# Optimization experiments

Hardware: AMD Instinct MI355X
Metric: run time of the kernel (lower is better)

Reference implementation:

```python
import jax, jax.numpy as jnp
import numpy as np

N = 200000   # active voxels
D = 80       # dense grid side
K = 27       # 3x3x3 kernel offsets
CIN, CMID, COUT = 16, 32, 32
EPS = 1e-3   # BatchNorm1d eps from the module


def _build_rulebook():
    """Submanifold conv rulebook: for each kernel offset, (input_idx, output_idx) pairs.
    Padded to length N with dummy output index N (scatter target discarded)."""
    rng = np.random.default_rng(0)
    lin = rng.choice(D ** 3, size=N, replace=False)
    coords = np.stack(np.unravel_index(lin, (D, D, D)), axis=1).astype(np.int64)  # [N,3]
    lookup = np.full(D ** 3, -1, np.int64)
    lookup[lin] = np.arange(N)
    rule_in = np.zeros((K, N), np.int32)
    rule_out = np.full((K, N), N, np.int32)  # dummy row N = padding
    k = 0
    for dx in (-1, 0, 1):
        for dy in (-1, 0, 1):
            for dz in (-1, 0, 1):
                nb = coords + np.array([dx, dy, dz])
                valid = np.all((nb >= 0) & (nb < D), axis=1)
                nb_lin = (nb[valid, 0] * D + nb[valid, 1]) * D + nb[valid, 2]
                idx = lookup[nb_lin]
                hit = idx >= 0
                src = idx[hit].astype(np.int32)
                dst = np.nonzero(valid)[0][hit].astype(np.int32)
                m = src.shape[0]
                rule_in[k, :m] = src
                rule_out[k, :m] = dst
                k += 1
    return rule_in, rule_out


def setup_inputs() -> dict:
    key = jax.random.key(0)
    ks = jax.random.split(key, 3)
    ri, ro = _build_rulebook()
    return {
        "feats": jax.random.normal(ks[0], (N, CIN), jnp.float32),
        "W1": jax.random.normal(ks[1], (K, CIN, CMID), jnp.float32) * 0.05,
        "gamma1": jnp.ones((CMID,), jnp.float32),
        "beta1": jnp.zeros((CMID,), jnp.float32),
        "W2": jax.random.normal(ks[2], (K, CMID, COUT), jnp.float32) * 0.05,
        "gamma2": jnp.ones((COUT,), jnp.float32),
        "beta2": jnp.zeros((COUT,), jnp.float32),
        "rule_in": jnp.asarray(ri),
        "rule_out": jnp.asarray(ro),
    }


def _subm_conv(feats, W, rule_in, rule_out):
    """Gather-GEMM-scatter over kernel offsets (lax.scan keeps one offset resident)."""
    n = feats.shape[0]

    def step(acc, xs):
        in_i, out_i, Wk = xs
        return acc.at[out_i].add(feats[in_i] @ Wk), None

    acc0 = jnp.zeros((n + 1, W.shape[-1]), feats.dtype)  # row n is padding sink
    acc, _ = jax.lax.scan(step, acc0, (rule_in, rule_out, W))
    return acc[:n]


def _bn_relu(x, gamma, beta):
    # BatchNorm1d training-mode forward (biased var) + ReLU
    mu = x.mean(0)
    var = jnp.mean((x - mu) ** 2, 0)
    return jax.nn.relu((x - mu) * jax.lax.rsqrt(var + EPS) * gamma + beta)


def reference(feats, W1, gamma1, beta1, W2, gamma2, beta2, rule_in, rule_out):
    x = _bn_relu(_subm_conv(feats, W1, rule_in, rule_out), gamma1, beta1)
    x = _bn_relu(_subm_conv(x, W2, rule_in, rule_out), gamma2, beta2)
    return x
```

## Files before the change

kernel.cpp:

```cpp
#include <hip/hip_runtime.h>

#define NVOX 200000
#define KOFF 27
#define CIN 16
#define CMID 32
#define COUT 32
#define EPSBN 1e-3f

typedef _Float16 f16x8 __attribute__((ext_vector_type(8)));
typedef _Float16 f16x4 __attribute__((ext_vector_type(4)));
typedef float f32x16 __attribute__((ext_vector_type(16)));

#define OFF_X1H 21600000
#define OFF_FH  34400064
#define OFF_WB1 40800096
#define OFF_WB2 40827744
#define OFF_ST  40883040

__global__ __launch_bounds__(256) void k_build(const int* __restrict__ rule_in,
                                               const int* __restrict__ rule_out,
                                               const float* __restrict__ feats,
                                               const float* __restrict__ W1,
                                               const float* __restrict__ W2,
                                               int* __restrict__ gatherT,
                                               _Float16* __restrict__ featsh,
                                               _Float16* __restrict__ WB1,
                                               _Float16* __restrict__ WB2,
                                               _Float16* __restrict__ x1h) {
  int e = blockIdx.x * 256 + threadIdx.x;
  if (e < KOFF * NVOX) {
    int k = e / NVOX;
    int dst = rule_out[e];
    if (dst < NVOX) gatherT[k * NVOX + dst] = rule_in[e];
  }
  if (e < NVOX * CIN / 4) {
    float4 f = ((const float4*)feats)[e];
    f16x4 h = {(_Float16)f.x, (_Float16)f.y, (_Float16)f.z, (_Float16)f.w};
    ((f16x4*)featsh)[e] = h;
  }
  if (e < KOFF * 512) {
    int j = e & 7, l = (e >> 3) & 63, k = e >> 9;
    int kk = ((l >> 5) << 3) + j;
    int n = l & 31;
    WB1[e] = (_Float16)W1[(k * CIN + kk) * CMID + n];
  }
  if (e < KOFF * 1024) {
    int j = e & 7, l = (e >> 3) & 63, f = (e >> 9) & 1, k = e >> 10;
    int kk = (f << 4) + ((l >> 5) << 3) + j;
    int n = l & 31;
    WB2[e] = (_Float16)W2[(k * CMID + kk) * COUT + n];
  }
  if (e < CMID) x1h[(size_t)NVOX * CMID + e] = (_Float16)0.f;
  if (e < CIN) featsh[(size_t)NVOX * CIN + e] = (_Float16)0.f;
}

__global__ __launch_bounds__(512, 4) void k_conv1m(const _Float16* __restrict__ featsh,
                                                   const int* __restrict__ gatherT,
                                                   const uint4* __restrict__ WB1,
                                                   _Float16* __restrict__ x1h,
                                                   float* __restrict__ gsums) {
  __shared__ uint4 wlds[KOFF * 64];
  __shared__ float lsum[64];
  int tid = threadIdx.x;
  for (int i = tid; i < KOFF * 64; i += 512) wlds[i] = WB1[i];
  if (tid < 64) lsum[tid] = 0.f;
  __syncthreads();

  int lane = tid & 63, wave = tid >> 6;
  int m = lane & 31, khalf = lane >> 5;
  int rowbase = blockIdx.x * 256 + wave * 32;
  int row = rowbase + m;
  int rowc = (row < NVOX) ? row : (NVOX - 1);

  int idx[KOFF];
#pragma unroll
  for (int k = 0; k < KOFF; ++k) idx[k] = gatherT[k * NVOX + rowc];

  f32x16 c;
#pragma unroll
  for (int i = 0; i < 16; ++i) c[i] = 0.f;

#pragma unroll
  for (int k = 0; k < KOFF; ++k) {
    unsigned s = ((unsigned)idx[k] < (unsigned)NVOX) ? (unsigned)idx[k] : (unsigned)NVOX;
    f16x8 a = *(const f16x8*)(featsh + (size_t)s * CIN + (khalf << 3));
    f16x8 b = ((const f16x8*)wlds)[k * 64 + lane];
    c = __builtin_amdgcn_mfma_f32_32x32x16_f16(a, b, c, 0, 0, 0);
  }

  float s0 = 0.f, q0 = 0.f;
#pragma unroll
  for (int r = 0; r < 16; ++r) {
    int grow = rowbase + (r & 3) + ((r >> 2) << 3) + (khalf << 2);
    float mk = (grow < NVOX) ? 1.f : 0.f;
    float v = c[r] * mk;
    s0 += v; q0 += v * v;
    if (grow < NVOX) x1h[(size_t)grow * CMID + m] = (_Float16)c[r];
  }
  s0 += __shfl_xor(s0, 32, 64);
  q0 += __shfl_xor(q0, 32, 64);
  if (lane < 32) {
    atomicAdd(&lsum[m], s0);
    atomicAdd(&lsum[32 + m], q0);
  }
  __syncthreads();
  if (tid < 64) atomicAdd(&gsums[tid], lsum[tid]);
}

__global__ __launch_bounds__(256) void k_bnrelu1h(_Float16* __restrict__ x1h,
                                                  const float* __restrict__ sums,
                                                  const float* __restrict__ gamma,
                                                  const float* __restrict__ beta) {
  int t = blockIdx.x * 256 + threadIdx.x;
  if (t >= NVOX * CMID / 8) return;
  int c = (t & 3) * 8;
  const float inv_n = 1.0f / (float)NVOX;
  float sc[8], sh[8];
#pragma unroll
  for (int i = 0; i < 8; ++i) {
    float mu = sums[c + i] * inv_n;
    float var = sums[32 + c + i] * inv_n - mu * mu;
    float s = gamma[c + i] * rsqrtf(var + EPSBN);
    sc[i] = s; sh[i] = beta[c + i] - mu * s;
  }
  f16x8* p = (f16x8*)x1h + t;
  f16x8 v = *p;
#pragma unroll
  for (int i = 0; i < 8; ++i) {
    float x = fmaf((float)v[i], sc[i], sh[i]);
    v[i] = (_Float16)fmaxf(x, 0.f);
  }
  *p = v;
}

__global__ __launch_bounds__(512, 4) void k_conv2m(const _Float16* __restrict__ x1h,
                                                   const int* __restrict__ gatherT,
                                                   const uint4* __restrict__ WB2,
                                                   float* __restrict__ out,
                                                   float* __restrict__ gsums) {
  __shared__ uint4 wlds[KOFF * 128];
  __shared__ float lsum[64];
  int tid = threadIdx.x;
  for (int i = tid; i < KOFF * 128; i += 512) wlds[i] = WB2[i];
  if (tid < 64) lsum[tid] = 0.f;
  __syncthreads();

  int lane = tid & 63, wave = tid >> 6;
  int m = lane & 31, khalf = lane >> 5;
  int rowbase = blockIdx.x * 256 + wave * 32;
  int row = rowbase + m;
  int rowc = (row < NVOX) ? row : (NVOX - 1);

  int idx[KOFF];
#pragma unroll
  for (int k = 0; k < KOFF; ++k) idx[k] = gatherT[k * NVOX + rowc];

  f32x16 c;
#pragma unroll
  for (int i = 0; i < 16; ++i) c[i] = 0.f;

#pragma unroll
  for (int k = 0; k < KOFF; ++k) {
    unsigned s = ((unsigned)idx[k] < (unsigned)NVOX) ? (unsigned)idx[k] : (unsigned)NVOX;
    const _Float16* rp = x1h + (size_t)s * CMID + (khalf << 3);
    f16x8 a0 = *(const f16x8*)(rp);
    f16x8 a1 = *(const f16x8*)(rp + 16);
    f16x8 b0 = ((const f16x8*)wlds)[(k * 2 + 0) * 64 + lane];
    f16x8 b1 = ((const f16x8*)wlds)[(k * 2 + 1) * 64 + lane];
    c = __builtin_amdgcn_mfma_f32_32x32x16_f16(a0, b0, c, 0, 0, 0);
    c = __builtin_amdgcn_mfma_f32_32x32x16_f16(a1, b1, c, 0, 0, 0);
  }

  float s0 = 0.f, q0 = 0.f;
#pragma unroll
  for (int r = 0; r < 16; ++r) {
    int grow = rowbase + (r & 3) + ((r >> 2) << 3) + (khalf << 2);
    float mk = (grow < NVOX) ? 1.f : 0.f;
    float v = c[r] * mk;
    s0 += v; q0 += v * v;
    if (grow < NVOX) out[(size_t)grow * COUT + m] = c[r];
  }
  s0 += __shfl_xor(s0, 32, 64);
  q0 += __shfl_xor(q0, 32, 64);
  if (lane < 32) {
    atomicAdd(&lsum[m], s0);
    atomicAdd(&lsum[32 + m], q0);
  }
  __syncthreads();
  if (tid < 64) atomicAdd(&gsums[tid], lsum[tid]);
}

__global__ __launch_bounds__(256) void k_bnrelu2(float* __restrict__ out,
                                                 const float* __restrict__ sums,
                                                 const float* __restrict__ gamma,
                                                 const float* __restrict__ beta) {
  int t = blockIdx.x * 256 + threadIdx.x;
  if (t >= NVOX * COUT / 4) return;
  int c = (t & 7) * 4;
  const float inv_n = 1.0f / (float)NVOX;
  float sc[4], sh[4];
#pragma unroll
  for (int i = 0; i < 4; ++i) {
    float mu = sums[c + i] * inv_n;
    float var = sums[32 + c + i] * inv_n - mu * mu;
    float s = gamma[c + i] * rsqrtf(var + EPSBN);
    sc[i] = s; sh[i] = beta[c + i] - mu * s;
  }
  float4* p = (float4*)out + t;
  float4 v = *p;
  v.x = fmaxf(fmaf(v.x, sc[0], sh[0]), 0.f);
  v.y = fmaxf(fmaf(v.y, sc[1], sh[1]), 0.f);
  v.z = fmaxf(fmaf(v.z, sc[2], sh[2]), 0.f);
  v.w = fmaxf(fmaf(v.w, sc[3], sh[3]), 0.f);
  *p = v;
}

extern "C" void kernel_launch(void* const* d_in, const int* in_sizes, int n_in,
                              void* d_out, int out_size, void* d_ws, size_t ws_size,
                              hipStream_t stream) {
  const float* feats  = (const float*)d_in[0];
  const float* W1     = (const float*)d_in[1];
  const float* gamma1 = (const float*)d_in[2];
  const float* beta1  = (const float*)d_in[3];
  const float* W2     = (const float*)d_in[4];
  const float* gamma2 = (const float*)d_in[5];
  const float* beta2  = (const float*)d_in[6];
  const int* rule_in  = (const int*)d_in[7];
  const int* rule_out = (const int*)d_in[8];
  float* out = (float*)d_out;

  int*       gatherT = (int*)d_ws;
  _Float16*  x1h     = (_Float16*)((char*)d_ws + OFF_X1H);
  _Float16*  featsh  = (_Float16*)((char*)d_ws + OFF_FH);
  _Float16*  WB1     = (_Float16*)((char*)d_ws + OFF_WB1);
  _Float16*  WB2     = (_Float16*)((char*)d_ws + OFF_WB2);
  float*     stats   = (float*)((char*)d_ws + OFF_ST);

  hipMemsetAsync(gatherT, 0xFF, (size_t)KOFF * NVOX * 4, stream);
  hipMemsetAsync(stats, 0, 128 * 4, stream);
  k_build<<<(KOFF * NVOX + 255) / 256, 256, 0, stream>>>(
      rule_in, rule_out, feats, W1, W2, gatherT, featsh, WB1, WB2, x1h);
  k_conv1m<<<782, 512, 0, stream>>>(featsh, gatherT, (const uint4*)WB1, x1h, stats);
  k_bnrelu1h<<<(NVOX * CMID / 8 + 255) / 256, 256, 0, stream>>>(x1h, stats, gamma1, beta1);
  k_conv2m<<<782, 512, 0, stream>>>(x1h, gatherT, (const uint4*)WB2, out, stats + 64);
  k_bnrelu2<<<(NVOX * COUT / 4 + 255) / 256, 256, 0, stream>>>(out, stats + 64, gamma2, beta2);
}
```

Measured before the change: 217.3 us.

## Fuse BN1+ReLU into conv2 gather, prefetch gathers, drop memsets

The first BatchNorm+ReLU pass is folded into conv2: it applies per-channel scale and shift in fp16 to the gathered rows and masks invalid neighbours, so the separate elementwise kernel and its read/write of x1h go away. Both conv kernels now prefetch gathered rows three offsets ahead through a small register ring, to hide gather latency. The memset of gatherT is replaced by filling -1 gaps in the build kernel, which assumes rule_out is sorted, and the stats memset moves into the build kernel as well. The costs are that the BN is recomputed 27 times per row in fp16, and the conv kernels need more registers.

```diff
diff --git a/kernel.cpp b/kernel.cpp
--- a/kernel.cpp
+++ b/kernel.cpp
@@ -26,12 +26,21 @@
                                                _Float16* __restrict__ featsh,
                                                _Float16* __restrict__ WB1,
                                                _Float16* __restrict__ WB2,
-                                               _Float16* __restrict__ x1h) {
+                                               float* __restrict__ stats) {
   int e = blockIdx.x * 256 + threadIdx.x;
   if (e < KOFF * NVOX) {
     int k = e / NVOX;
+    int pos = e - k * NVOX;
     int dst = rule_out[e];
-    if (dst < NVOX) gatherT[k * NVOX + dst] = rule_in[e];
+    int ndst = (pos == NVOX - 1) ? NVOX : rule_out[e + 1];
+    int* __restrict__ gk = gatherT + k * NVOX;
+    if (dst < NVOX) {
+      gk[dst] = rule_in[e];
+      if (pos == 0) {
+        for (int d = 0; d < dst; ++d) gk[d] = -1;
+      }
+      for (int d = dst + 1; d < ndst; ++d) gk[d] = -1;
+    }
   }
   if (e < NVOX * CIN / 4) {
     float4 f = ((const float4*)feats)[e];
@@ -50,8 +59,8 @@
     int n = l & 31;
     WB2[e] = (_Float16)W2[(k * CMID + kk) * COUT + n];
   }
-  if (e < CMID) x1h[(size_t)NVOX * CMID + e] = (_Float16)0.f;
   if (e < CIN) featsh[(size_t)NVOX * CIN + e] = (_Float16)0.f;
+  if (e < 128) stats[e] = 0.f;
 }
 
 __global__ __launch_bounds__(512, 4) void k_conv1m(const _Float16* __restrict__ featsh,
@@ -67,7 +76,7 @@
   __syncthreads();
 
   int lane = tid & 63, wave = tid >> 6;
-  int m = lane & 31, khalf = lane >> 5;
+  int m = lane & 31, h = lane >> 5;
   int rowbase = blockIdx.x * 256 + wave * 32;
   int row = rowbase + m;
   int rowc = (row < NVOX) ? row : (NVOX - 1);
@@ -76,14 +85,24 @@
 #pragma unroll
   for (int k = 0; k < KOFF; ++k) idx[k] = gatherT[k * NVOX + rowc];
 
+  f16x8 A[3];
+#pragma unroll
+  for (int p = 0; p < 3; ++p) {
+    unsigned s = ((unsigned)idx[p] < (unsigned)NVOX) ? (unsigned)idx[p] : (unsigned)NVOX;
+    A[p] = *(const f16x8*)(featsh + (size_t)s * CIN + (h << 3));
+  }
+
   f32x16 c;
 #pragma unroll
   for (int i = 0; i < 16; ++i) c[i] = 0.f;
 
 #pragma unroll
   for (int k = 0; k < KOFF; ++k) {
-    unsigned s = ((unsigned)idx[k] < (unsigned)NVOX) ? (unsigned)idx[k] : (unsigned)NVOX;
-    f16x8 a = *(const f16x8*)(featsh + (size_t)s * CIN + (khalf << 3));
+    f16x8 a = A[k % 3];
+    if (k + 3 < KOFF) {
+      unsigned s = ((unsigned)idx[k + 3] < (unsigned)NVOX) ? (unsigned)idx[k + 3] : (unsigned)NVOX;
+      A[k % 3] = *(const f16x8*)(featsh + (size_t)s * CIN + (h << 3));
+    }
     f16x8 b = ((const f16x8*)wlds)[k * 64 + lane];
     c = __builtin_amdgcn_mfma_f32_32x32x16_f16(a, b, c, 0, 0, 0);
   }
@@ -91,7 +110,7 @@
   float s0 = 0.f, q0 = 0.f;
 #pragma unroll
   for (int r = 0; r < 16; ++r) {
-    int grow = rowbase + (r & 3) + ((r >> 2) << 3) + (khalf << 2);
+    int grow = rowbase + (r & 3) + ((r >> 2) << 3) + (h << 2);
     float mk = (grow < NVOX) ? 1.f : 0.f;
     float v = c[r] * mk;
     s0 += v; q0 += v * v;
@@ -107,35 +126,12 @@
   if (tid < 64) atomicAdd(&gsums[tid], lsum[tid]);
 }
 
-__global__ __launch_bounds__(256) void k_bnrelu1h(_Float16* __restrict__ x1h,
-                                                  const float* __restrict__ sums,
-                                                  const float* __restrict__ gamma,
-                                                  const float* __restrict__ beta) {
-  int t = blockIdx.x * 256 + threadIdx.x;
-  if (t >= NVOX * CMID / 8) return;
-  int c = (t & 3) * 8;
-  const float inv_n = 1.0f / (float)NVOX;
-  float sc[8], sh[8];
-#pragma unroll
-  for (int i = 0; i < 8; ++i) {
-    float mu = sums[c + i] * inv_n;
-    float var = sums[32 + c + i] * inv_n - mu * mu;
-    float s = gamma[c + i] * rsqrtf(var + EPSBN);
-    sc[i] = s; sh[i] = beta[c + i] - mu * s;
-  }
-  f16x8* p = (f16x8*)x1h + t;
-  f16x8 v = *p;
-#pragma unroll
-  for (int i = 0; i < 8; ++i) {
-    float x = fmaf((float)v[i], sc[i], sh[i]);
-    v[i] = (_Float16)fmaxf(x, 0.f);
-  }
-  *p = v;
-}
-
 __global__ __launch_bounds__(512, 4) void k_conv2m(const _Float16* __restrict__ x1h,
                                                    const int* __restrict__ gatherT,
                                                    const uint4* __restrict__ WB2,
+                                                   const float* __restrict__ sums1,
+                                                   const float* __restrict__ gamma1,
+                                                   const float* __restrict__ beta1,
                                                    float* __restrict__ out,
                                                    float* __restrict__ gsums) {
   __shared__ uint4 wlds[KOFF * 128];
@@ -146,35 +142,75 @@
   __syncthreads();
 
   int lane = tid & 63, wave = tid >> 6;
-  int m = lane & 31, khalf = lane >> 5;
+  int m = lane & 31, h = lane >> 5;
   int rowbase = blockIdx.x * 256 + wave * 32;
   int row = rowbase + m;
   int rowc = (row < NVOX) ? row : (NVOX - 1);
 
+  const float inv_n = 1.0f / (float)NVOX;
+  f16x8 sc0, sh0, sc1, sh1;
+#pragma unroll
+  for (int i = 0; i < 8; ++i) {
+    int c0 = 8 * h + i;
+    float mu = sums1[c0] * inv_n;
+    float var = sums1[32 + c0] * inv_n - mu * mu;
+    float s = gamma1[c0] * rsqrtf(var + EPSBN);
+    sc0[i] = (_Float16)s; sh0[i] = (_Float16)(beta1[c0] - mu * s);
+    int c1 = 16 + 8 * h + i;
+    mu = sums1[c1] * inv_n;
+    var = sums1[32 + c1] * inv_n - mu * mu;
+    s = gamma1[c1] * rsqrtf(var + EPSBN);
+    sc1[i] = (_Float16)s; sh1[i] = (_Float16)(beta1[c1] - mu * s);
+  }
+
   int idx[KOFF];
 #pragma unroll
   for (int k = 0; k < KOFF; ++k) idx[k] = gatherT[k * NVOX + rowc];
 
+  f16x8 A0[3], A1[3];
+#pragma unroll
+  for (int p = 0; p < 3; ++p) {
+    unsigned s = ((unsigned)idx[p] < (unsigned)NVOX) ? (unsigned)idx[p] : 0u;
+    const _Float16* rp = x1h + (size_t)s * CMID + (h << 3);
+    A0[p] = *(const f16x8*)rp;
+    A1[p] = *(const f16x8*)(rp + 16);
+  }
+
   f32x16 c;
 #pragma unroll
   for (int i = 0; i < 16; ++i) c[i] = 0.f;
 
+  const _Float16 zero_h = (_Float16)0.f;
 #pragma unroll
   for (int k = 0; k < KOFF; ++k) {
-    unsigned s = ((unsigned)idx[k] < (unsigned)NVOX) ? (unsigned)idx[k] : (unsigned)NVOX;
-    const _Float16* rp = x1h + (size_t)s * CMID + (khalf << 3);
-    f16x8 a0 = *(const f16x8*)(rp);
-    f16x8 a1 = *(const f16x8*)(rp + 16);
+    _Float16 mk = ((unsigned)idx[k] < (unsigned)NVOX) ? (_Float16)1.f : zero_h;
+    f16x8 a0 = A0[k % 3], a1 = A1[k % 3];
+    f16x8 y0, y1;
+#pragma unroll
+    for (int i = 0; i < 8; ++i) {
+      _Float16 t0 = a0[i] * sc0[i] + sh0[i];
+      t0 = (t0 > zero_h) ? t0 : zero_h;
+      y0[i] = t0 * mk;
+      _Float16 t1 = a1[i] * sc1[i] + sh1[i];
+      t1 = (t1 > zero_h) ? t1 : zero_h;
+      y1[i] = t1 * mk;
+    }
+    if (k + 3 < KOFF) {
+      unsigned s = ((unsigned)idx[k + 3] < (unsigned)NVOX) ? (unsigned)idx[k + 3] : 0u;
+      const _Float16* rp = x1h + (size_t)s * CMID + (h << 3);
+      A0[k % 3] = *(const f16x8*)rp;
+      A1[k % 3] = *(const f16x8*)(rp + 16);
+    }
     f16x8 b0 = ((const f16x8*)wlds)[(k * 2 + 0) * 64 + lane];
     f16x8 b1 = ((const f16x8*)wlds)[(k * 2 + 1) * 64 + lane];
-    c = __builtin_amdgcn_mfma_f32_32x32x16_f16(a0, b0, c, 0, 0, 0);
-    c = __builtin_amdgcn_mfma_f32_32x32x16_f16(a1, b1, c, 0, 0, 0);
+    c = __builtin_amdgcn_mfma_f32_32x32x16_f16(y0, b0, c, 0, 0, 0);
+    c = __builtin_amdgcn_mfma_f32_32x32x16_f16(y1, b1, c, 0, 0, 0);
   }
 
   float s0 = 0.f, q0 = 0.f;
 #pragma unroll
   for (int r = 0; r < 16; ++r) {
-    int grow = rowbase + (r & 3) + ((r >> 2) << 3) + (khalf << 2);
+    int grow = rowbase + (r & 3) + ((r >> 2) << 3) + (h << 2);
     float mk = (grow < NVOX) ? 1.f : 0.f;
     float v = c[r] * mk;
     s0 += v; q0 += v * v;
@@ -236,12 +272,10 @@
   _Float16*  WB2     = (_Float16*)((char*)d_ws + OFF_WB2);
   float*     stats   = (float*)((char*)d_ws + OFF_ST);
 
-  hipMemsetAsync(gatherT, 0xFF, (size_t)KOFF * NVOX * 4, stream);
-  hipMemsetAsync(stats, 0, 128 * 4, stream);
   k_build<<<(KOFF * NVOX + 255) / 256, 256, 0, stream>>>(
-      rule_in, rule_out, feats, W1, W2, gatherT, featsh, WB1, WB2, x1h);
+      rule_in, rule_out, feats, W1, W2, gatherT, featsh, WB1, WB2, stats);
   k_conv1m<<<782, 512, 0, stream>>>(featsh, gatherT, (const uint4*)WB1, x1h, stats);
-  k_bnrelu1h<<<(NVOX * CMID / 8 + 255) / 256, 256, 0, stream>>>(x1h, stats, gamma1, beta1);
-  k_conv2m<<<782, 512, 0, stream>>>(x1h, gatherT, (const uint4*)WB2, out, stats + 64);
+  k_conv2m<<<782, 512, 0, stream>>>(x1h, gatherT, (const uint4*)WB2,
+                                    stats, gamma1, beta1, out, stats + 64);
   k_bnrelu2<<<(NVOX * COUT / 4 + 255) / 256, 256, 0, stream>>>(out, stats + 64, gamma2, beta2);
 }
```

New measurement: 218.2 us. About the same (+0.5%).

## Drop gather-table memset and software-pipeline feature gathers in conv kernels

Applied to the files above, without the earlier changes.

Removes the large hipMemsetAsync over the gather table by having k_build fill the -1 gaps between consecutive rule_out destinations. This relies on rule_out being sorted within each offset. Stats zeroing moves into k_build too. Both conv kernels now keep a register ring of prefetched gathered rows (depth 8 for conv1, 6 for conv2) so global gathers are issued several MFMAs ahead, at the cost of more VGPRs under a tight launch bound.

```diff
diff --git a/kernel.cpp b/kernel.cpp
--- a/kernel.cpp
+++ b/kernel.cpp
@@ -6,6 +6,8 @@
 #define CMID 32
 #define COUT 32
 #define EPSBN 1e-3f
+#define PD1 8
+#define PD2 6
 
 typedef _Float16 f16x8 __attribute__((ext_vector_type(8)));
 typedef _Float16 f16x4 __attribute__((ext_vector_type(4)));
@@ -26,12 +28,22 @@
                                                _Float16* __restrict__ featsh,
                                                _Float16* __restrict__ WB1,
                                                _Float16* __restrict__ WB2,
-                                               _Float16* __restrict__ x1h) {
+                                               _Float16* __restrict__ x1h,
+                                               float* __restrict__ stats) {
   int e = blockIdx.x * 256 + threadIdx.x;
   if (e < KOFF * NVOX) {
     int k = e / NVOX;
+    int pos = e - k * NVOX;
     int dst = rule_out[e];
-    if (dst < NVOX) gatherT[k * NVOX + dst] = rule_in[e];
+    int ndst = (pos == NVOX - 1) ? NVOX : rule_out[e + 1];
+    int* __restrict__ gk = gatherT + k * NVOX;
+    if (dst < NVOX) {
+      gk[dst] = rule_in[e];
+      if (pos == 0) {
+        for (int d = 0; d < dst; ++d) gk[d] = -1;
+      }
+      for (int d = dst + 1; d < ndst; ++d) gk[d] = -1;
+    }
   }
   if (e < NVOX * CIN / 4) {
     float4 f = ((const float4*)feats)[e];
@@ -50,8 +62,9 @@
     int n = l & 31;
     WB2[e] = (_Float16)W2[(k * CMID + kk) * COUT + n];
   }
+  if (e < CIN) featsh[(size_t)NVOX * CIN + e] = (_Float16)0.f;
   if (e < CMID) x1h[(size_t)NVOX * CMID + e] = (_Float16)0.f;
-  if (e < CIN) featsh[(size_t)NVOX * CIN + e] = (_Float16)0.f;
+  if (e < 128) stats[e] = 0.f;
 }
 
 __global__ __launch_bounds__(512, 4) void k_conv1m(const _Float16* __restrict__ featsh,
@@ -67,7 +80,7 @@
   __syncthreads();
 
   int lane = tid & 63, wave = tid >> 6;
-  int m = lane & 31, khalf = lane >> 5;
+  int m = lane & 31, h = lane >> 5;
   int rowbase = blockIdx.x * 256 + wave * 32;
   int row = rowbase + m;
   int rowc = (row < NVOX) ? row : (NVOX - 1);
@@ -76,14 +89,24 @@
 #pragma unroll
   for (int k = 0; k < KOFF; ++k) idx[k] = gatherT[k * NVOX + rowc];
 
+  f16x8 A[PD1];
+#pragma unroll
+  for (int p = 0; p < PD1; ++p) {
+    unsigned s = ((unsigned)idx[p] < (unsigned)NVOX) ? (unsigned)idx[p] : (unsigned)NVOX;
+    A[p] = *(const f16x8*)(featsh + (size_t)s * CIN + (h << 3));
+  }
+
   f32x16 c;
 #pragma unroll
   for (int i = 0; i < 16; ++i) c[i] = 0.f;
 
 #pragma unroll
   for (int k = 0; k < KOFF; ++k) {
-    unsigned s = ((unsigned)idx[k] < (unsigned)NVOX) ? (unsigned)idx[k] : (unsigned)NVOX;
-    f16x8 a = *(const f16x8*)(featsh + (size_t)s * CIN + (khalf << 3));
+    f16x8 a = A[k % PD1];
+    if (k + PD1 < KOFF) {
+      unsigned s = ((unsigned)idx[k + PD1] < (unsigned)NVOX) ? (unsigned)idx[k + PD1] : (unsigned)NVOX;
+      A[k % PD1] = *(const f16x8*)(featsh + (size_t)s * CIN + (h << 3));
+    }
     f16x8 b = ((const f16x8*)wlds)[k * 64 + lane];
     c = __builtin_amdgcn_mfma_f32_32x32x16_f16(a, b, c, 0, 0, 0);
   }
@@ -91,7 +114,7 @@
   float s0 = 0.f, q0 = 0.f;
 #pragma unroll
   for (int r = 0; r < 16; ++r) {
-    int grow = rowbase + (r & 3) + ((r >> 2) << 3) + (khalf << 2);
+    int grow = rowbase + (r & 3) + ((r >> 2) << 3) + (h << 2);
     float mk = (grow < NVOX) ? 1.f : 0.f;
     float v = c[r] * mk;
     s0 += v; q0 += v * v;
@@ -146,7 +169,7 @@
   __syncthreads();
 
   int lane = tid & 63, wave = tid >> 6;
-  int m = lane & 31, khalf = lane >> 5;
+  int m = lane & 31, h = lane >> 5;
   int rowbase = blockIdx.x * 256 + wave * 32;
   int row = rowbase + m;
   int rowc = (row < NVOX) ? row : (NVOX - 1);
@@ -155,16 +178,28 @@
 #pragma unroll
   for (int k = 0; k < KOFF; ++k) idx[k] = gatherT[k * NVOX + rowc];
 
+  f16x8 A0[PD2], A1[PD2];
+#pragma unroll
+  for (int p = 0; p < PD2; ++p) {
+    unsigned s = ((unsigned)idx[p] < (unsigned)NVOX) ? (unsigned)idx[p] : (unsigned)NVOX;
+    const _Float16* rp = x1h + (size_t)s * CMID + (h << 3);
+    A0[p] = *(const f16x8*)rp;
+    A1[p] = *(const f16x8*)(rp + 16);
+  }
+
   f32x16 c;
 #pragma unroll
   for (int i = 0; i < 16; ++i) c[i] = 0.f;
 
 #pragma unroll
   for (int k = 0; k < KOFF; ++k) {
-    unsigned s = ((unsigned)idx[k] < (unsigned)NVOX) ? (unsigned)idx[k] : (unsigned)NVOX;
-    const _Float16* rp = x1h + (size_t)s * CMID + (khalf << 3);
-    f16x8 a0 = *(const f16x8*)(rp);
-    f16x8 a1 = *(const f16x8*)(rp + 16);
+    f16x8 a0 = A0[k % PD2], a1 = A1[k % PD2];
+    if (k + PD2 < KOFF) {
+      unsigned s = ((unsigned)idx[k + PD2] < (unsigned)NVOX) ? (unsigned)idx[k + PD2] : (unsigned)NVOX;
+      const _Float16* rp = x1h + (size_t)s * CMID + (h << 3);
+      A0[k % PD2] = *(const f16x8*)rp;
+      A1[k % PD2] = *(const f16x8*)(rp + 16);
+    }
     f16x8 b0 = ((const f16x8*)wlds)[(k * 2 + 0) * 64 + lane];
     f16x8 b1 = ((const f16x8*)wlds)[(k * 2 + 1) * 64 + lane];
     c = __builtin_amdgcn_mfma_f32_32x32x16_f16(a0, b0, c, 0, 0, 0);
@@ -174,7 +209,7 @@
   float s0 = 0.f, q0 = 0.f;
 #pragma unroll
   for (int r = 0; r < 16; ++r) {
-    int grow = rowbase + (r & 3) + ((r >> 2) << 3) + (khalf << 2);
+    int grow = rowbase + (r & 3) + ((r >> 2) << 3) + (h << 2);
     float mk = (grow < NVOX) ? 1.f : 0.f;
     float v = c[r] * mk;
     s0 += v; q0 += v * v;
@@ -236,10 +271,8 @@
   _Float16*  WB2     = (_Float16*)((char*)d_ws + OFF_WB2);
   float*     stats   = (float*)((char*)d_ws + OFF_ST);
 
-  hipMemsetAsync(gatherT, 0xFF, (size_t)KOFF * NVOX * 4, stream);
-  hipMemsetAsync(stats, 0, 128 * 4, stream);
   k_build<<<(KOFF * NVOX + 255) / 256, 256, 0, stream>>>(
-      rule_in, rule_out, feats, W1, W2, gatherT, featsh, WB1, WB2, x1h);
+      rule_in, rule_out, feats, W1, W2, gatherT, featsh, WB1, WB2, x1h, stats);
   k_conv1m<<<782, 512, 0, stream>>>(featsh, gatherT, (const uint4*)WB1, x1h, stats);
   k_bnrelu1h<<<(NVOX * CMID / 8 + 255) / 256, 256, 0, stream>>>(x1h, stats, gamma1, beta1);
   k_conv2m<<<782, 512, 0, stream>>>(x1h, gatherT, (const uint4*)WB2, out, stats + 64);
```

After: 208.8 us. -3.9%, faster.
